# Kernel tuning notes

Hardware: AMD Instinct MI355X
Metric: run time of the kernel (lower is better)

## Reference

```python
import jax, jax.numpy as jnp
import numpy as np

NX = 2048
NL = 20
BATCH = 512
EIGMAX = 10.0
EPS = 1e-9


def prox_cardan(eta, x):
    """Prox of u -> -eta*(log(u)+log(1-u)) at x: unique root in (0,1) of
    u^3 - (1+x)u^2 + (x-2eta)u + eta = 0 (Cardano / trigonometric method)."""
    b = -(1.0 + x)
    c = x - 2.0 * eta
    d = eta
    p = c - b * b / 3.0
    q = 2.0 * b ** 3 / 27.0 - b * c / 3.0 + d
    disc = -4.0 * p ** 3 - 27.0 * q ** 2
    # three-real-roots branch (trigonometric); requires p<0
    pm = jnp.minimum(p, -1e-12)
    m = 2.0 * jnp.sqrt(-pm / 3.0)
    arg = jnp.clip(3.0 * q / (pm * m), -1.0, 1.0)
    th = jnp.arccos(arg)
    k = jnp.arange(3, dtype=x.dtype)
    t_trig = m[..., None] * jnp.cos((th[..., None] - 2.0 * jnp.pi * k) / 3.0)
    r_trig = t_trig - b[..., None] / 3.0
    in01 = (r_trig > 0.0) & (r_trig < 1.0)
    idx = jnp.argmax(in01, axis=-1)
    root3 = jnp.take_along_axis(r_trig, idx[..., None], axis=-1)[..., 0]
    # one-real-root branch
    s = jnp.sqrt(jnp.maximum(q * q / 4.0 + p ** 3 / 27.0, 0.0))
    root1 = jnp.cbrt(-q / 2.0 + s) + jnp.cbrt(-q / 2.0 - s) - b / 3.0
    u = jnp.where(disc >= 0.0, root3, root1)
    return jnp.clip(u, EPS, 1.0 - EPS)


def setup_inputs() -> dict:
    key = jax.random.key(0)
    k1, k2, k3, k4, k5 = jax.random.split(key, 5)
    x = jax.random.uniform(k1, (BATCH, 1, NX), dtype=jnp.float32)
    # symmetric PSD operators for T^T T and D^T D (as in a discretized inverse problem)
    A = jax.random.normal(k2, (NX, NX), dtype=jnp.float32)
    tTT = (A @ A.T) / NX
    B = jax.random.normal(k3, (NX, NX), dtype=jnp.float32)
    tDD = (B @ B.T) / NX
    # orthogonal change-of-basis: element <-> eigen bases
    Q, _ = jnp.linalg.qr(jax.random.normal(k4, (NX, NX), dtype=jnp.float32))
    Pelt = Q.astype(jnp.float32)
    Peig = Q.T.astype(jnp.float32)
    x_b = jnp.einsum('ij,bcj->bci', tTT, x) + 0.01 * jax.random.normal(k5, (BATCH, 1, NX), dtype=jnp.float32)
    gamma = jnp.full((NL,), 0.1, dtype=jnp.float32)   # nn.Parameter([0.1])
    mu = jnp.zeros((NL,), dtype=jnp.float32)          # nn.Parameter([0.0])
    reg = jnp.full((NL,), 0.001, dtype=jnp.float32)   # noisy=True -> trainable 0.001
    return {"x": x, "x_b": x_b, "tDD": tDD, "tTT": tTT, "Peig": Peig,
            "Pelt": Pelt, "gamma": gamma, "mu": mu, "reg": reg}


def reference(x, x_b, tDD, tTT, Peig, Pelt, gamma, mu, reg):
    def step(xc, params):
        g_raw, mu_raw, reg_raw = params
        g = jax.nn.softplus(g_raw)
        mu_l = jax.nn.softplus(mu_raw) / 1e6
        reg_l = jax.nn.softplus(reg_raw) / (EIGMAX ** 2)
        grad = (jnp.einsum('ij,bcj->bci', tTT, xc) - x_b
                + reg_l * jnp.einsum('ij,bcj->bci', tDD, xc))
        xt = xc - g * grad
        xt = jnp.einsum('ij,bcj->bci', Pelt, xt)
        xt = prox_cardan(g * mu_l, xt)
        xt = jnp.einsum('ij,bcj->bci', Peig, xt)
        return xt, None

    out, _ = jax.lax.scan(step, x, (gamma, mu, reg))
    return out
```

## Files before the change

### kernel.cpp

```cpp
#include <hip/hip_runtime.h>
#include <math.h>

#define MDIM 512
#define NDIM 2048
#define KDIM 2048
#define NLAYERS 20

static const size_t MN = (size_t)MDIM * NDIM;
static const size_t OPN = (size_t)KDIM * KDIM;

using bf16x8 = __attribute__((ext_vector_type(8))) short;
using f32x4  = __attribute__((ext_vector_type(4))) float;

__device__ __forceinline__ double softplusd(double v) {
    return (v > 20.0) ? v : log1p(exp(v));
}

__device__ __forceinline__ float prox_cardan_f(float eta, float x) {
    const float b  = -(1.0f + x);
    const float c  = x - 2.0f * eta;
    const float dd = eta;
    const float p  = c - b * b * (1.0f / 3.0f);
    const float q  = 2.0f * b * b * b * (1.0f / 27.0f) - b * c * (1.0f / 3.0f) + dd;
    const float disc = -4.0f * p * p * p - 27.0f * q * q;
    const float pm = fminf(p, -1e-12f);
    const float mm = 2.0f * sqrtf(-pm * (1.0f / 3.0f));
    float arg = 3.0f * q / (pm * mm);
    arg = fminf(fmaxf(arg, -1.0f), 1.0f);
    const float th = acosf(arg);
    const float TWO_PI = 6.28318530717958647692f;
    const float r0 = mm * cosf(th * (1.0f / 3.0f)) - b * (1.0f / 3.0f);
    const float r1 = mm * cosf((th - TWO_PI) * (1.0f / 3.0f)) - b * (1.0f / 3.0f);
    const float r2 = mm * cosf((th - 2.0f * TWO_PI) * (1.0f / 3.0f)) - b * (1.0f / 3.0f);
    const bool in0 = (r0 > 0.0f) && (r0 < 1.0f);
    const bool in1 = (r1 > 0.0f) && (r1 < 1.0f);
    const bool in2 = (r2 > 0.0f) && (r2 < 1.0f);
    const float root3 = in0 ? r0 : (in1 ? r1 : (in2 ? r2 : r0));
    const float s = sqrtf(fmaxf(q * q * 0.25f + p * p * p * (1.0f / 27.0f), 0.0f));
    const float root1 = cbrtf(-q * 0.5f + s) + cbrtf(-q * 0.5f - s) - b * (1.0f / 3.0f);
    const float u = (disc >= 0.0f) ? root3 : root1;
    return fminf(fmaxf(u, 1e-9f), 1.0f - 1e-9f);
}

__device__ __forceinline__ double prox_newton_d(double eta, double x) {
    double u = (double)prox_cardan_f((float)eta, (float)x);
#pragma unroll
    for (int i = 0; i < 4; ++i) {
        const double um1 = u - 1.0;
        const double umx = u - x;
        const double P  = u * um1 * umx - eta * (2.0 * u - 1.0);
        const double dP = um1 * umx + u * umx + u * um1 - 2.0 * eta;
        u = u - P / dP;
        u = fmin(fmax(u, 1e-12), 1.0 - 1e-12);
    }
    return fmin(fmax(u, 1e-9), 1.0 - 1e-9);
}

__device__ __forceinline__ unsigned short f2bf(float f) {
    unsigned u = __float_as_uint(f);
    unsigned r = (u + 0x7FFFu + ((u >> 16) & 1u)) >> 16;
    return (unsigned short)r;
}
__device__ __forceinline__ float bf2f(unsigned short h) {
    return __uint_as_float(((unsigned)h) << 16);
}
__device__ __forceinline__ void split3f(float f, unsigned short& b1,
                                        unsigned short& b2, unsigned short& b3) {
    b1 = f2bf(f);
    const float r1 = f - bf2f(b1);
    b2 = f2bf(r1);
    const float r2 = r1 - bf2f(b2);
    b3 = f2bf(r2);
}

__global__ __launch_bounds__(256) void split3_op(
    const float* __restrict__ s1, const float* __restrict__ s2,
    const float* __restrict__ greg, int layer,
    unsigned short* __restrict__ p1, unsigned short* __restrict__ p2,
    unsigned short* __restrict__ p3) {
    const size_t i = ((size_t)blockIdx.x * 256 + threadIdx.x) * 4;
    float reglf = 0.0f;
    if (s2) reglf = (float)(softplusd((double)greg[layer]) * 0.01);
    const float4 a = *(const float4*)(s1 + i);
    float4 b = make_float4(0.f, 0.f, 0.f, 0.f);
    if (s2) b = *(const float4*)(s2 + i);
    ushort4 o1, o2, o3;
    split3f(fmaf(reglf, b.x, a.x), o1.x, o2.x, o3.x);
    split3f(fmaf(reglf, b.y, a.y), o1.y, o2.y, o3.y);
    split3f(fmaf(reglf, b.z, a.z), o1.z, o2.z, o3.z);
    split3f(fmaf(reglf, b.w, a.w), o1.w, o2.w, o3.w);
    *(ushort4*)(p1 + i) = o1;
    *(ushort4*)(p2 + i) = o2;
    *(ushort4*)(p3 + i) = o3;
}

__global__ __launch_bounds__(256) void split3_w(
    const float* __restrict__ s1, const float* __restrict__ s2,
    const float* __restrict__ greg, int layer,
    unsigned short* __restrict__ p1, unsigned short* __restrict__ p2,
    unsigned short* __restrict__ p3) {
    if (layer > 0 && greg[layer] == greg[0]) return;
    const size_t i = ((size_t)blockIdx.x * 256 + threadIdx.x) * 4;
    const float reglf = (float)(softplusd((double)greg[layer]) * 0.01);
    const float4 a = *(const float4*)(s1 + i);
    const float4 b = *(const float4*)(s2 + i);
    ushort4 o1, o2, o3;
    split3f(fmaf(reglf, b.x, a.x), o1.x, o2.x, o3.x);
    split3f(fmaf(reglf, b.y, a.y), o1.y, o2.y, o3.y);
    split3f(fmaf(reglf, b.z, a.z), o1.z, o2.z, o3.z);
    split3f(fmaf(reglf, b.w, a.w), o1.w, o2.w, o3.w);
    *(ushort4*)(p1 + i) = o1;
    *(ushort4*)(p2 + i) = o2;
    *(ushort4*)(p3 + i) = o3;
}

__global__ __launch_bounds__(256, 3) void gemm_bf16x3(
    const unsigned short* __restrict__ A1, const unsigned short* __restrict__ A2,
    const unsigned short* __restrict__ A3,
    const unsigned short* __restrict__ W1, const unsigned short* __restrict__ W2,
    const unsigned short* __restrict__ W3,
    float* __restrict__ Part, int klen) {
    __shared__ __align__(16) unsigned short Ab[3][64][32];
    __shared__ __align__(16) unsigned short Wb[3][64][32];

    const int tid = threadIdx.x;
    const int n0 = blockIdx.x * 64;
    const int m0 = blockIdx.y * 64;
    const int kb = blockIdx.z * klen;
    const int lane = tid & 63, wid = tid >> 6;
    const int quad = lane >> 4, lrow = lane & 15;
    const int wm = (wid >> 1) * 32, wn = (wid & 1) * 32;

    const int srow = tid >> 2;
    const int skc  = (tid & 3) * 8;

    const unsigned short* gA1 = A1 + (size_t)(m0 + srow) * KDIM + kb + skc;
    const unsigned short* gA2 = A2 + (size_t)(m0 + srow) * KDIM + kb + skc;
    const unsigned short* gA3 = A3 + (size_t)(m0 + srow) * KDIM + kb + skc;
    const unsigned short* gW1 = W1 + (size_t)(n0 + srow) * KDIM + kb + skc;
    const unsigned short* gW2 = W2 + (size_t)(n0 + srow) * KDIM + kb + skc;
    const unsigned short* gW3 = W3 + (size_t)(n0 + srow) * KDIM + kb + skc;

    bf16x8 sa1 = *(const bf16x8*)gA1, sa2 = *(const bf16x8*)gA2, sa3 = *(const bf16x8*)gA3;
    bf16x8 sw1 = *(const bf16x8*)gW1, sw2 = *(const bf16x8*)gW2, sw3 = *(const bf16x8*)gW3;

    f32x4 ahi[2][2], alo[2][2];
#pragma unroll
    for (int a = 0; a < 2; ++a)
#pragma unroll
        for (int b = 0; b < 2; ++b) {
            ahi[a][b] = (f32x4){0.f, 0.f, 0.f, 0.f};
            alo[a][b] = (f32x4){0.f, 0.f, 0.f, 0.f};
        }

    for (int k0 = 0; k0 < klen; k0 += 32) {
        *(bf16x8*)&Ab[0][srow][skc] = sa1;
        *(bf16x8*)&Ab[1][srow][skc] = sa2;
        *(bf16x8*)&Ab[2][srow][skc] = sa3;
        *(bf16x8*)&Wb[0][srow][skc] = sw1;
        *(bf16x8*)&Wb[1][srow][skc] = sw2;
        *(bf16x8*)&Wb[2][srow][skc] = sw3;
        __syncthreads();

        if (k0 + 32 < klen) {
            sa1 = *(const bf16x8*)(gA1 + k0 + 32);
            sa2 = *(const bf16x8*)(gA2 + k0 + 32);
            sa3 = *(const bf16x8*)(gA3 + k0 + 32);
            sw1 = *(const bf16x8*)(gW1 + k0 + 32);
            sw2 = *(const bf16x8*)(gW2 + k0 + 32);
            sw3 = *(const bf16x8*)(gW3 + k0 + 32);
        }

        bf16x8 fa[2][3], fw[2][3];
#pragma unroll
        for (int t = 0; t < 2; ++t) {
            const int ra = wm + t * 16 + lrow;
            const int rw = wn + t * 16 + lrow;
            fa[t][0] = *(const bf16x8*)&Ab[0][ra][quad * 8];
            fa[t][1] = *(const bf16x8*)&Ab[1][ra][quad * 8];
            fa[t][2] = *(const bf16x8*)&Ab[2][ra][quad * 8];
            fw[t][0] = *(const bf16x8*)&Wb[0][rw][quad * 8];
            fw[t][1] = *(const bf16x8*)&Wb[1][rw][quad * 8];
            fw[t][2] = *(const bf16x8*)&Wb[2][rw][quad * 8];
        }
#pragma unroll
        for (int tm = 0; tm < 2; ++tm)
#pragma unroll
            for (int tn = 0; tn < 2; ++tn) {
                ahi[tm][tn] = __builtin_amdgcn_mfma_f32_16x16x32_bf16(fa[tm][0], fw[tn][0], ahi[tm][tn], 0, 0, 0);
                alo[tm][tn] = __builtin_amdgcn_mfma_f32_16x16x32_bf16(fa[tm][0], fw[tn][1], alo[tm][tn], 0, 0, 0);
                alo[tm][tn] = __builtin_amdgcn_mfma_f32_16x16x32_bf16(fa[tm][1], fw[tn][0], alo[tm][tn], 0, 0, 0);
                alo[tm][tn] = __builtin_amdgcn_mfma_f32_16x16x32_bf16(fa[tm][1], fw[tn][1], alo[tm][tn], 0, 0, 0);
                alo[tm][tn] = __builtin_amdgcn_mfma_f32_16x16x32_bf16(fa[tm][0], fw[tn][2], alo[tm][tn], 0, 0, 0);
                alo[tm][tn] = __builtin_amdgcn_mfma_f32_16x16x32_bf16(fa[tm][2], fw[tn][0], alo[tm][tn], 0, 0, 0);
            }
        __syncthreads();
    }

    float* P = Part + (size_t)blockIdx.z * MN;
#pragma unroll
    for (int tm = 0; tm < 2; ++tm)
#pragma unroll
        for (int tn = 0; tn < 2; ++tn) {
            const int mbase = m0 + wm + tm * 16 + quad * 4;
            const int nn = n0 + wn + tn * 16 + lrow;
#pragma unroll
            for (int r = 0; r < 4; ++r)
                P[(size_t)(mbase + r) * NDIM + nn] = ahi[tm][tn][r] + alo[tm][tn][r];
        }
}

template <int MODE>
__global__ __launch_bounds__(256) void combine3(
    const float* __restrict__ Part, int S,
    const float* __restrict__ Xc, const float* __restrict__ Xb,
    float* __restrict__ stateOut,
    unsigned short* __restrict__ p1, unsigned short* __restrict__ p2,
    unsigned short* __restrict__ p3,
    const float* __restrict__ gam, const float* __restrict__ gmu,
    const float* __restrict__ greg, int layer) {
    const size_t i = ((size_t)blockIdx.x * 256 + threadIdx.x) * 4;
    double s0 = 0.0, s1 = 0.0, s2 = 0.0, s3 = 0.0;
    for (int z = 0; z < S; ++z) {
        const float4 p = *(const float4*)(Part + (size_t)z * MN + i);
        s0 += (double)p.x; s1 += (double)p.y; s2 += (double)p.z; s3 += (double)p.w;
    }
    float v0, v1, v2, v3;
    if (MODE == 0) {
        const double g = softplusd((double)gam[layer]);
        const float4 xc = *(const float4*)(Xc + i);
        const float4 xb = *(const float4*)(Xb + i);
        v0 = (float)((double)xc.x - g * (s0 - (double)xb.x));
        v1 = (float)((double)xc.y - g * (s1 - (double)xb.y));
        v2 = (float)((double)xc.z - g * (s2 - (double)xb.z));
        v3 = (float)((double)xc.w - g * (s3 - (double)xb.w));
    } else if (MODE == 1) {
        const double g   = softplusd((double)gam[layer]);
        const double eta = g * softplusd((double)gmu[layer]) * 1e-6;
        v0 = (float)prox_newton_d(eta, s0);
        v1 = (float)prox_newton_d(eta, s1);
        v2 = (float)prox_newton_d(eta, s2);
        v3 = (float)prox_newton_d(eta, s3);
    } else {
        v0 = (float)s0; v1 = (float)s1; v2 = (float)s2; v3 = (float)s3;
        *(float4*)(stateOut + i) = make_float4(v0, v1, v2, v3);
    }
    ushort4 o1, o2, o3;
    split3f(v0, o1.x, o2.x, o3.x);
    split3f(v1, o1.y, o2.y, o3.y);
    split3f(v2, o1.z, o2.z, o3.z);
    split3f(v3, o1.w, o2.w, o3.w);
    *(ushort4*)(p1 + i) = o1;
    *(ushort4*)(p2 + i) = o2;
    *(ushort4*)(p3 + i) = o3;
}

#define BM 64
#define BN 64
#define BK 32
#define LDSP 68

__device__ __forceinline__ double prox_cardan_d(double eta, double x) {
    const double b  = -(1.0 + x);
    const double c  = x - 2.0 * eta;
    const double dd = eta;
    const double p  = c - b * b * (1.0 / 3.0);
    const double q  = 2.0 * b * b * b * (1.0 / 27.0) - b * c * (1.0 / 3.0) + dd;
    const double disc = -4.0 * p * p * p - 27.0 * q * q;
    const double pm = fmin(p, -1e-12);
    const double mm = 2.0 * sqrt(-pm * (1.0 / 3.0));
    double arg = 3.0 * q / (pm * mm);
    arg = fmin(fmax(arg, -1.0), 1.0);
    const double th = acos(arg);
    const double TWO_PI = 6.283185307179586476925286766559;
    const double r0 = mm * cos(th * (1.0 / 3.0)) - b * (1.0 / 3.0);
    const double r1 = mm * cos((th - TWO_PI) * (1.0 / 3.0)) - b * (1.0 / 3.0);
    const double r2 = mm * cos((th - 2.0 * TWO_PI) * (1.0 / 3.0)) - b * (1.0 / 3.0);
    const bool in0 = (r0 > 0.0) && (r0 < 1.0);
    const bool in1 = (r1 > 0.0) && (r1 < 1.0);
    const bool in2 = (r2 > 0.0) && (r2 < 1.0);
    const double root3 = in0 ? r0 : (in1 ? r1 : (in2 ? r2 : r0));
    const double s = sqrt(fmax(q * q * 0.25 + p * p * p * (1.0 / 27.0), 0.0));
    const double root1 = cbrt(-q * 0.5 + s) + cbrt(-q * 0.5 - s) - b * (1.0 / 3.0);
    const double u = (disc >= 0.0) ? root3 : root1;
    return fmin(fmax(u, 1e-9), 1.0 - 1e-9);
}

template <bool FUSE2>
__global__ __launch_bounds__(256, 4) void gemm_nt_splitk(
    const float* __restrict__ A, const float* __restrict__ W1,
    const float* __restrict__ W2, double* __restrict__ Part,
    const float* __restrict__ greg, int layer, int klen) {
    __shared__ float As[BK][LDSP];
    __shared__ float Ws[BK][LDSP];
    const int tid = threadIdx.x;
    const int m0 = blockIdx.y * BM;
    const int n0 = blockIdx.x * BN;
    const int kbase = blockIdx.z * klen;
    float reglf = 0.0f;
    if (FUSE2) reglf = (float)(softplusd((double)greg[layer]) * 0.01);
    const int lrow = tid >> 3;
    const int lkc  = (tid & 7) << 2;
    const float* pA  = A  + (size_t)(m0 + lrow) * KDIM + kbase + lkc;
    const float* pW  = W1 + (size_t)(n0 + lrow) * KDIM + kbase + lkc;
    const float* pW2 = FUSE2 ? (W2 + (size_t)(n0 + lrow) * KDIM + kbase + lkc) : nullptr;
    float4 ra[2], rw[2];
    ra[0] = *(const float4*)(pA);
    ra[1] = *(const float4*)(pA + 32 * KDIM);
    rw[0] = *(const float4*)(pW);
    rw[1] = *(const float4*)(pW + 32 * KDIM);
    if (FUSE2) {
        const float4 u0 = *(const float4*)(pW2);
        const float4 u1 = *(const float4*)(pW2 + 32 * KDIM);
        rw[0].x += reglf * u0.x; rw[0].y += reglf * u0.y;
        rw[0].z += reglf * u0.z; rw[0].w += reglf * u0.w;
        rw[1].x += reglf * u1.x; rw[1].y += reglf * u1.y;
        rw[1].z += reglf * u1.z; rw[1].w += reglf * u1.w;
    }
    float  acc[4][4]   = {};
    double acc64[4][4] = {};
    const int tx = (tid & 15) << 2;
    const int ty = (tid >> 4) << 2;
    int it = 0;
    for (int k0 = 0; k0 < klen; k0 += BK, ++it) {
#pragma unroll
        for (int h = 0; h < 2; ++h) {
            const int row = lrow + (h << 5);
            As[lkc + 0][row] = (h ? ra[1].x : ra[0].x);
            As[lkc + 1][row] = (h ? ra[1].y : ra[0].y);
            As[lkc + 2][row] = (h ? ra[1].z : ra[0].z);
            As[lkc + 3][row] = (h ? ra[1].w : ra[0].w);
            Ws[lkc + 0][row] = (h ? rw[1].x : rw[0].x);
            Ws[lkc + 1][row] = (h ? rw[1].y : rw[0].y);
            Ws[lkc + 2][row] = (h ? rw[1].z : rw[0].z);
            Ws[lkc + 3][row] = (h ? rw[1].w : rw[0].w);
        }
        __syncthreads();
        if (k0 + BK < klen) {
            const float* qA = pA + k0 + BK;
            ra[0] = *(const float4*)(qA);
            ra[1] = *(const float4*)(qA + 32 * KDIM);
            const float* qW = pW + k0 + BK;
            rw[0] = *(const float4*)(qW);
            rw[1] = *(const float4*)(qW + 32 * KDIM);
            if (FUSE2) {
                const float* qW2 = pW2 + k0 + BK;
                const float4 u0 = *(const float4*)(qW2);
                const float4 u1 = *(const float4*)(qW2 + 32 * KDIM);
                rw[0].x += reglf * u0.x; rw[0].y += reglf * u0.y;
                rw[0].z += reglf * u0.z; rw[0].w += reglf * u0.w;
                rw[1].x += reglf * u1.x; rw[1].y += reglf * u1.y;
                rw[1].z += reglf * u1.z; rw[1].w += reglf * u1.w;
            }
        }
#pragma unroll
        for (int kk = 0; kk < BK; ++kk) {
            const float4 a4 = *(const float4*)(&As[kk][ty]);
            const float4 b4 = *(const float4*)(&Ws[kk][tx]);
            const float av[4] = {a4.x, a4.y, a4.z, a4.w};
            const float bv[4] = {b4.x, b4.y, b4.z, b4.w};
#pragma unroll
            for (int r = 0; r < 4; ++r)
#pragma unroll
                for (int cc = 0; cc < 4; ++cc)
                    acc[r][cc] = fmaf(av[r], bv[cc], acc[r][cc]);
        }
        __syncthreads();
        if ((it & 1) == 1) {
#pragma unroll
            for (int r = 0; r < 4; ++r)
#pragma unroll
                for (int cc = 0; cc < 4; ++cc) {
                    acc64[r][cc] += (double)acc[r][cc];
                    acc[r][cc] = 0.0f;
                }
        }
    }
#pragma unroll
    for (int r = 0; r < 4; ++r)
#pragma unroll
        for (int cc = 0; cc < 4; ++cc)
            acc64[r][cc] += (double)acc[r][cc];
    double* Pz = Part + (size_t)blockIdx.z * MN;
#pragma unroll
    for (int r = 0; r < 4; ++r) {
        double* q = Pz + (size_t)(m0 + ty + r) * NDIM + n0 + tx;
        *(double2*)(q)     = make_double2(acc64[r][0], acc64[r][1]);
        *(double2*)(q + 2) = make_double2(acc64[r][2], acc64[r][3]);
    }
}

template <int MODE>
__global__ __launch_bounds__(256) void combine_ep(
    const double* __restrict__ Part, int nslices,
    const float* __restrict__ Xc, const float* __restrict__ Xb,
    float* __restrict__ Out,
    const float* __restrict__ gam, const float* __restrict__ gmu,
    const float* __restrict__ greg, int layer) {
    const size_t i4 = ((size_t)blockIdx.x * 256 + threadIdx.x) * 4;
    double s0 = 0.0, s1 = 0.0, s2 = 0.0, s3 = 0.0;
    for (int z = 0; z < nslices; ++z) {
        const double* p = Part + (size_t)z * MN + i4;
        const double2 a = *(const double2*)(p);
        const double2 b = *(const double2*)(p + 2);
        s0 += a.x; s1 += a.y; s2 += b.x; s3 += b.y;
    }
    float4 o;
    if (MODE == 0) {
        const double g = softplusd((double)gam[layer]);
        const float4 xc = *(const float4*)(Xc + i4);
        const float4 xb = *(const float4*)(Xb + i4);
        o.x = (float)((double)xc.x - g * (s0 - (double)xb.x));
        o.y = (float)((double)xc.y - g * (s1 - (double)xb.y));
        o.z = (float)((double)xc.z - g * (s2 - (double)xb.z));
        o.w = (float)((double)xc.w - g * (s3 - (double)xb.w));
    } else if (MODE == 1) {
        const double g   = softplusd((double)gam[layer]);
        const double eta = g * softplusd((double)gmu[layer]) * 1e-6;
        o.x = (float)prox_cardan_d(eta, s0);
        o.y = (float)prox_cardan_d(eta, s1);
        o.z = (float)prox_cardan_d(eta, s2);
        o.w = (float)prox_cardan_d(eta, s3);
    } else {
        o.x = (float)s0; o.y = (float)s1; o.z = (float)s2; o.w = (float)s3;
    }
    *(float4*)(Out + i4) = o;
}

extern "C" void kernel_launch(void* const* d_in, const int* in_sizes, int n_in,
                              void* d_out, int out_size, void* d_ws, size_t ws_size,
                              hipStream_t stream) {
    const float* x    = (const float*)d_in[0];
    const float* x_b  = (const float*)d_in[1];
    const float* tDD  = (const float*)d_in[2];
    const float* tTT  = (const float*)d_in[3];
    const float* Peig = (const float*)d_in[4];
    const float* Pelt = (const float*)d_in[5];
    const float* gam  = (const float*)d_in[6];
    const float* gmu  = (const float*)d_in[7];
    const float* greg = (const float*)d_in[8];
    float* out = (float*)d_out;

    const size_t TRI_OP_B = 3 * OPN * 2;
    const size_t TRI_A_B  = 3 * MN * 2;
    const size_t STATE_B  = MN * 4;
    const size_t full_need = 3 * TRI_OP_B + 2 * TRI_A_B + STATE_B + 2 * MN * 4;
    const size_t mid_need  = 1 * TRI_OP_B + 2 * TRI_A_B + STATE_B + 2 * MN * 4;

    const bool full = (ws_size >= full_need);
    const bool mid  = (!full && ws_size >= mid_need);

    if (full || mid) {
        const int S = 2;
        const int klen = KDIM / S;
        char* p = (char*)d_ws;
        unsigned short *Wt1, *Wt2, *Wt3, *Pe1, *Pe2, *Pe3, *Pg1, *Pg2, *Pg3;
        if (full) {
            Wt1 = (unsigned short*)p;        Wt2 = Wt1 + OPN; Wt3 = Wt2 + OPN; p += TRI_OP_B;
            Pe1 = (unsigned short*)p;        Pe2 = Pe1 + OPN; Pe3 = Pe2 + OPN; p += TRI_OP_B;
            Pg1 = (unsigned short*)p;        Pg2 = Pg1 + OPN; Pg3 = Pg2 + OPN; p += TRI_OP_B;
        } else {
            Wt1 = (unsigned short*)p;        Wt2 = Wt1 + OPN; Wt3 = Wt2 + OPN; p += TRI_OP_B;
            Pe1 = Wt1; Pe2 = Wt2; Pe3 = Wt3;
            Pg1 = Wt1; Pg2 = Wt2; Pg3 = Wt3;
        }
        unsigned short* Aa1 = (unsigned short*)p; unsigned short* Aa2 = Aa1 + MN;
        unsigned short* Aa3 = Aa2 + MN; p += TRI_A_B;
        unsigned short* Ab1 = (unsigned short*)p; unsigned short* Ab2 = Ab1 + MN;
        unsigned short* Ab3 = Ab2 + MN; p += TRI_A_B;
        float* state = (float*)p; p += STATE_B;
        float* part  = (float*)p;

        const dim3 gg(NDIM / 64, MDIM / 64, S);
        const unsigned cgrid = (unsigned)(MN / 4 / 256);
        const unsigned ogrid = (unsigned)(OPN / 4 / 256);

        split3_op<<<cgrid, 256, 0, stream>>>(x, nullptr, greg, 0, Aa1, Aa2, Aa3);
        if (full) {
            split3_op<<<ogrid, 256, 0, stream>>>(Pelt, nullptr, greg, 0, Pe1, Pe2, Pe3);
            split3_op<<<ogrid, 256, 0, stream>>>(Peig, nullptr, greg, 0, Pg1, Pg2, Pg3);
        }

        unsigned short *c1 = Aa1, *c2 = Aa2, *c3 = Aa3;
        unsigned short *d1 = Ab1, *d2 = Ab2, *d3 = Ab3;

        for (int l = 0; l < NLAYERS; ++l) {
            if (full) {
                split3_w<<<ogrid, 256, 0, stream>>>(tTT, tDD, greg, l, Wt1, Wt2, Wt3);
            } else {
                split3_op<<<ogrid, 256, 0, stream>>>(tTT, tDD, greg, l, Wt1, Wt2, Wt3);
            }
            gemm_bf16x3<<<gg, 256, 0, stream>>>(c1, c2, c3, Wt1, Wt2, Wt3, part, klen);
            combine3<0><<<cgrid, 256, 0, stream>>>(part, S, (l == 0 ? x : state), x_b,
                                                   nullptr, d1, d2, d3, gam, gmu, greg, l);
            if (mid) split3_op<<<ogrid, 256, 0, stream>>>(Pelt, nullptr, greg, 0, Pe1, Pe2, Pe3);
            gemm_bf16x3<<<gg, 256, 0, stream>>>(d1, d2, d3, Pe1, Pe2, Pe3, part, klen);
            combine3<1><<<cgrid, 256, 0, stream>>>(part, S, nullptr, nullptr,
                                                   nullptr, c1, c2, c3, gam, gmu, greg, l);
            if (mid) split3_op<<<ogrid, 256, 0, stream>>>(Peig, nullptr, greg, 0, Pg1, Pg2, Pg3);
            gemm_bf16x3<<<gg, 256, 0, stream>>>(c1, c2, c3, Pg1, Pg2, Pg3, part, klen);
            combine3<2><<<cgrid, 256, 0, stream>>>(part, S, nullptr, nullptr,
                                                   (l == NLAYERS - 1 ? out : state),
                                                   d1, d2, d3, gam, gmu, greg, l);
            unsigned short* t;
            t = c1; c1 = d1; d1 = t;
            t = c2; c2 = d2; d2 = t;
            t = c3; c3 = d3; d3 = t;
        }
        return;
    }

    char* wsb = (char*)d_ws;
    float* b0 = (float*)wsb;
    float* b1 = b0 + MN;
    float* b2 = b1 + MN;
    float* b3 = b2 + MN;
    const size_t base_bytes = 4 * MN * sizeof(float);
    double* partd = (double*)(wsb + base_bytes);
    int S = 0;
    if (ws_size >= base_bytes + 2 * MN * sizeof(double)) S = 2;
    else if (ws_size >= base_bytes + 1 * MN * sizeof(double)) S = 1;
    if (S == 0) return;
    const int klen = KDIM / S;
    dim3 gg(NDIM / BN, MDIM / BM, S);
    dim3 cg((unsigned)(MN / 4 / 256));
    const float* cur = x;
    float* bx = b0; float* bu = b1; float* bn = b2; float* bo = b3;
    for (int l = 0; l < NLAYERS; ++l) {
        gemm_nt_splitk<true><<<gg, 256, 0, stream>>>(cur, tTT, tDD, partd, greg, l, klen);
        combine_ep<0><<<cg, 256, 0, stream>>>(partd, S, cur, x_b, bx, gam, gmu, greg, l);
        gemm_nt_splitk<false><<<gg, 256, 0, stream>>>(bx, Pelt, nullptr, partd, greg, l, klen);
        combine_ep<1><<<cg, 256, 0, stream>>>(partd, S, nullptr, nullptr, bu, gam, gmu, greg, l);
        gemm_nt_splitk<false><<<gg, 256, 0, stream>>>(bu, Peig, nullptr, partd, greg, l, klen);
        float* dst = (l == NLAYERS - 1) ? out : bn;
        combine_ep<2><<<cg, 256, 0, stream>>>(partd, S, nullptr, nullptr, dst, gam, gmu, greg, l);
        cur = bn;
        float* t = bn; bn = bo; bo = t;
    }
}
```

Baseline: 2.616 ms.

## Double-buffer GEMM LDS tiles with direct global-to-LDS loads

```diff
diff --git a/kernel.cpp b/kernel.cpp
--- a/kernel.cpp
+++ b/kernel.cpp
@@ -73,6 +73,12 @@
     b3 = f2bf(r2);
 }
 
+__device__ __forceinline__ void glds16(const unsigned short* g, unsigned short* l) {
+    __builtin_amdgcn_global_load_lds(
+        (const __attribute__((address_space(1))) unsigned int*)g,
+        (__attribute__((address_space(3))) unsigned int*)l, 16, 0, 0);
+}
+
 __global__ __launch_bounds__(256) void split3_op(
     const float* __restrict__ s1, const float* __restrict__ s2,
     const float* __restrict__ greg, int layer,
@@ -114,14 +120,14 @@
     *(ushort4*)(p3 + i) = o3;
 }
 
-__global__ __launch_bounds__(256, 3) void gemm_bf16x3(
+__global__ __launch_bounds__(256, 2) void gemm_bf16x3_v5(
     const unsigned short* __restrict__ A1, const unsigned short* __restrict__ A2,
     const unsigned short* __restrict__ A3,
     const unsigned short* __restrict__ W1, const unsigned short* __restrict__ W2,
     const unsigned short* __restrict__ W3,
     float* __restrict__ Part, int klen) {
-    __shared__ __align__(16) unsigned short Ab[3][64][32];
-    __shared__ __align__(16) unsigned short Wb[3][64][32];
+    __shared__ __align__(16) unsigned short Ab[2][3][64][32];
+    __shared__ __align__(16) unsigned short Wb[2][3][64][32];
 
     const int tid = threadIdx.x;
     const int n0 = blockIdx.x * 64;
@@ -131,8 +137,9 @@
     const int quad = lane >> 4, lrow = lane & 15;
     const int wm = (wid >> 1) * 32, wn = (wid & 1) * 32;
 
-    const int srow = tid >> 2;
-    const int skc  = (tid & 3) * 8;
+    const int srow = (wid << 4) + (lane >> 2);
+    const int skc  = (lane & 3) * 8;
+    const int lrow0 = wid << 4;
 
     const unsigned short* gA1 = A1 + (size_t)(m0 + srow) * KDIM + kb + skc;
     const unsigned short* gA2 = A2 + (size_t)(m0 + srow) * KDIM + kb + skc;
@@ -141,8 +148,12 @@
     const unsigned short* gW2 = W2 + (size_t)(n0 + srow) * KDIM + kb + skc;
     const unsigned short* gW3 = W3 + (size_t)(n0 + srow) * KDIM + kb + skc;
 
-    bf16x8 sa1 = *(const bf16x8*)gA1, sa2 = *(const bf16x8*)gA2, sa3 = *(const bf16x8*)gA3;
-    bf16x8 sw1 = *(const bf16x8*)gW1, sw2 = *(const bf16x8*)gW2, sw3 = *(const bf16x8*)gW3;
+    glds16(gA1, &Ab[0][0][srow][skc]);
+    glds16(gA2, &Ab[0][1][srow][skc]);
+    glds16(gA3, &Ab[0][2][srow][skc]);
+    glds16(gW1, &Wb[0][0][srow][skc]);
+    glds16(gW2, &Wb[0][1][srow][skc]);
+    glds16(gW3, &Wb[0][2][srow][skc]);
 
     f32x4 ahi[2][2], alo[2][2];
 #pragma unroll
@@ -153,22 +164,19 @@
             alo[a][b] = (f32x4){0.f, 0.f, 0.f, 0.f};
         }
 
+    int cur = 0;
     for (int k0 = 0; k0 < klen; k0 += 32) {
-        *(bf16x8*)&Ab[0][srow][skc] = sa1;
-        *(bf16x8*)&Ab[1][srow][skc] = sa2;
-        *(bf16x8*)&Ab[2][srow][skc] = sa3;
-        *(bf16x8*)&Wb[0][srow][skc] = sw1;
-        *(bf16x8*)&Wb[1][srow][skc] = sw2;
-        *(bf16x8*)&Wb[2][srow][skc] = sw3;
         __syncthreads();
 
         if (k0 + 32 < klen) {
-            sa1 = *(const bf16x8*)(gA1 + k0 + 32);
-            sa2 = *(const bf16x8*)(gA2 + k0 + 32);
-            sa3 = *(const bf16x8*)(gA3 + k0 + 32);
-            sw1 = *(const bf16x8*)(gW1 + k0 + 32);
-            sw2 = *(const bf16x8*)(gW2 + k0 + 32);
-            sw3 = *(const bf16x8*)(gW3 + k0 + 32);
+            const int nb = cur ^ 1;
+            const int ko = k0 + 32;
+            glds16(gA1 + ko, &Ab[nb][0][srow][skc]);
+            glds16(gA2 + ko, &Ab[nb][1][srow][skc]);
+            glds16(gA3 + ko, &Ab[nb][2][srow][skc]);
+            glds16(gW1 + ko, &Wb[nb][0][srow][skc]);
+            glds16(gW2 + ko, &Wb[nb][1][srow][skc]);
+            glds16(gW3 + ko, &Wb[nb][2][srow][skc]);
         }
 
         bf16x8 fa[2][3], fw[2][3];
@@ -176,12 +184,12 @@
         for (int t = 0; t < 2; ++t) {
             const int ra = wm + t * 16 + lrow;
             const int rw = wn + t * 16 + lrow;
-            fa[t][0] = *(const bf16x8*)&Ab[0][ra][quad * 8];
-            fa[t][1] = *(const bf16x8*)&Ab[1][ra][quad * 8];
-            fa[t][2] = *(const bf16x8*)&Ab[2][ra][quad * 8];
-            fw[t][0] = *(const bf16x8*)&Wb[0][rw][quad * 8];
-            fw[t][1] = *(const bf16x8*)&Wb[1][rw][quad * 8];
-            fw[t][2] = *(const bf16x8*)&Wb[2][rw][quad * 8];
+            fa[t][0] = *(const bf16x8*)&Ab[cur][0][ra][quad * 8];
+            fa[t][1] = *(const bf16x8*)&Ab[cur][1][ra][quad * 8];
+            fa[t][2] = *(const bf16x8*)&Ab[cur][2][ra][quad * 8];
+            fw[t][0] = *(const bf16x8*)&Wb[cur][0][rw][quad * 8];
+            fw[t][1] = *(const bf16x8*)&Wb[cur][1][rw][quad * 8];
+            fw[t][2] = *(const bf16x8*)&Wb[cur][2][rw][quad * 8];
         }
 #pragma unroll
         for (int tm = 0; tm < 2; ++tm)
@@ -194,7 +202,7 @@
                 alo[tm][tn] = __builtin_amdgcn_mfma_f32_16x16x32_bf16(fa[tm][0], fw[tn][2], alo[tm][tn], 0, 0, 0);
                 alo[tm][tn] = __builtin_amdgcn_mfma_f32_16x16x32_bf16(fa[tm][2], fw[tn][0], alo[tm][tn], 0, 0, 0);
             }
-        __syncthreads();
+        cur ^= 1;
     }
 
     float* P = Part + (size_t)blockIdx.z * MN;
@@ -490,15 +498,15 @@
             } else {
                 split3_op<<<ogrid, 256, 0, stream>>>(tTT, tDD, greg, l, Wt1, Wt2, Wt3);
             }
-            gemm_bf16x3<<<gg, 256, 0, stream>>>(c1, c2, c3, Wt1, Wt2, Wt3, part, klen);
+            gemm_bf16x3_v5<<<gg, 256, 0, stream>>>(c1, c2, c3, Wt1, Wt2, Wt3, part, klen);
             combine3<0><<<cgrid, 256, 0, stream>>>(part, S, (l == 0 ? x : state), x_b,
                                                    nullptr, d1, d2, d3, gam, gmu, greg, l);
             if (mid) split3_op<<<ogrid, 256, 0, stream>>>(Pelt, nullptr, greg, 0, Pe1, Pe2, Pe3);
-            gemm_bf16x3<<<gg, 256, 0, stream>>>(d1, d2, d3, Pe1, Pe2, Pe3, part, klen);
+            gemm_bf16x3_v5<<<gg, 256, 0, stream>>>(d1, d2, d3, Pe1, Pe2, Pe3, part, klen);
             combine3<1><<<cgrid, 256, 0, stream>>>(part, S, nullptr, nullptr,
                                                    nullptr, c1, c2, c3, gam, gmu, greg, l);
             if (mid) split3_op<<<ogrid, 256, 0, stream>>>(Peig, nullptr, greg, 0, Pg1, Pg2, Pg3);
-            gemm_bf16x3<<<gg, 256, 0, stream>>>(c1, c2, c3, Pg1, Pg2, Pg3, part, klen);
+            gemm_bf16x3_v5<<<gg, 256, 0, stream>>>(c1, c2, c3, Pg1, Pg2, Pg3, part, klen);
             combine3<2><<<cgrid, 256, 0, stream>>>(part, S, nullptr, nullptr,
                                                    (l == NLAYERS - 1 ? out : state),
                                                    d1, d2, d3, gam, gmu, greg, l);
```

Measured after the change: 2.725 ms. 1.04x slower.
